# Performance work log

Hardware: AMD Instinct MI355X
Metric: run time of the kernel (lower is better)

## Reference

```python
import jax, jax.numpy as jnp
import numpy as np

N, E, D, L = 20000, 320000, 3072, 64
H = D // 2  # 1536
EPS = 1e-5


def setup_inputs() -> dict:
    key = jax.random.key(0)
    ks = jax.random.split(key, 16)
    inp = {
        "x": jax.random.normal(ks[0], (N, D), dtype=jnp.float32),
        "edge_index": jax.random.randint(ks[1], (2, E), 0, N, dtype=jnp.int64),
        # GCNConv weights (x @ W + b)
        "W_gc1": jax.random.normal(ks[2], (D, H), dtype=jnp.float32) / np.sqrt(D),
        "b_gc1": jnp.zeros((H,), dtype=jnp.float32),
        "W_gc2": jax.random.normal(ks[3], (H, L), dtype=jnp.float32) / np.sqrt(H),
        "b_gc2": jnp.zeros((L,), dtype=jnp.float32),
        # LayerNorm params
        "g1": jnp.ones((H,), dtype=jnp.float32),
        "be1": jnp.zeros((H,), dtype=jnp.float32),
        "g2": jnp.ones((L,), dtype=jnp.float32),
        "be2": jnp.zeros((L,), dtype=jnp.float32),
        # Decoder Linears (PyTorch: y = x @ W.T + b; store as [in, out])
        "W_fc1": jax.random.normal(ks[4], (L, H), dtype=jnp.float32) / np.sqrt(L),
        "b_fc1": jnp.zeros((H,), dtype=jnp.float32),
        "W_fc2": jax.random.normal(ks[5], (H, D), dtype=jnp.float32) / np.sqrt(H),
        "b_fc2": jnp.zeros((D,), dtype=jnp.float32),
    }
    return inp


def _layernorm(h, g, b):
    mu = jnp.mean(h, axis=-1, keepdims=True)
    var = jnp.mean(jnp.square(h - mu), axis=-1, keepdims=True)
    return (h - mu) * jax.lax.rsqrt(var + EPS) * g + b


def _gcn_norm(edge_index, n):
    # PyG GCNConv default: add self-loops, symmetric normalization
    loop = jnp.arange(n, dtype=edge_index.dtype)
    src = jnp.concatenate([edge_index[0], loop])  # [E+N]
    dst = jnp.concatenate([edge_index[1], loop])
    deg = jax.ops.segment_sum(jnp.ones_like(dst, dtype=jnp.float32), dst, num_segments=n)
    dinv = jax.lax.rsqrt(jnp.maximum(deg, 1e-12))
    norm = dinv[src] * dinv[dst]  # [E+N]
    return src, dst, norm


def _gcn_conv(h, W, b, src, dst, norm, n):
    h = h @ W                                 # [N, out]
    m = h[src] * norm[:, None]                # gather + scale over edges
    out = jax.ops.segment_sum(m, dst, num_segments=n)  # scatter-add
    return out + b


def reference(x, edge_index, W_gc1, b_gc1, W_gc2, b_gc2, g1, be1, g2, be2,
              W_fc1, b_fc1, W_fc2, b_fc2):
    n = x.shape[0]
    src, dst, norm = _gcn_norm(edge_index, n)
    hidden = jax.nn.relu(_gcn_conv(x, W_gc1, b_gc1, src, dst, norm, n))
    hidden = _layernorm(hidden, g1, be1)
    latent = jax.nn.relu(_gcn_conv(hidden, W_gc2, b_gc2, src, dst, norm, n))
    latent = _layernorm(latent, g2, be2)
    decode = jax.nn.relu(latent @ W_fc1 + b_fc1)
    reconstructed = decode @ W_fc2 + b_fc2
    return latent, reconstructed
```

## Files before the change

### kernel.cpp

```cpp
#include <hip/hip_runtime.h>
#include <hip/hip_bf16.h>

#define NN 20000
#define EE 320000
#define DD 3072
#define HH 1536
#define LL 64

typedef unsigned short bf16_t;
typedef __attribute__((ext_vector_type(8))) __bf16 bf16x8;
typedef __attribute__((ext_vector_type(4))) float  f32x4;

__device__ __forceinline__ bf16_t f2bf(float f) {
    union { float f; unsigned u; } c; c.f = f;
    unsigned u = c.u;
    return (bf16_t)((u + 0x7fffu + ((u >> 16) & 1u)) >> 16);
}

__global__ void zero_int(int* __restrict__ p, int n) {
    int i = blockIdx.x * blockDim.x + threadIdx.x;
    if (i < n) p[i] = 0;
}

__global__ void cnt_count(const int* __restrict__ ei, int* __restrict__ cnt, int E) {
    int i = blockIdx.x * blockDim.x + threadIdx.x;
    if (i < E) atomicAdd(&cnt[ei[E + i]], 1);
}

__global__ void dinv_from_cnt(const int* __restrict__ cnt, float* __restrict__ dinv, int n) {
    int i = blockIdx.x * blockDim.x + threadIdx.x;
    if (i < n) dinv[i] = rsqrtf((float)(cnt[i] + 1));
}

__global__ __launch_bounds__(1024) void scan_rowptr(const int* __restrict__ cnt,
                                                    int* __restrict__ rowptr, int n)
{
    __shared__ int sdata[1024];
    __shared__ int scarry;
    const int tid = threadIdx.x;
    if (tid == 0) scarry = 0;
    __syncthreads();
    for (int base = 0; base < n; base += 1024) {
        int i = base + tid;
        int v = (i < n) ? cnt[i] : 0;
        int x = v;
        sdata[tid] = x;
        __syncthreads();
#pragma unroll
        for (int off = 1; off < 1024; off <<= 1) {
            int y = (tid >= off) ? sdata[tid - off] : 0;
            __syncthreads();
            x += y;
            sdata[tid] = x;
            __syncthreads();
        }
        if (i < n) rowptr[i] = scarry + x - v;
        int total = sdata[1023];
        __syncthreads();
        if (tid == 0) scarry += total;
        __syncthreads();
    }
    if (tid == 0) rowptr[n] = scarry;
}

__global__ void csr_fill(const int* __restrict__ ei, const int* __restrict__ rowptr,
                         int* __restrict__ cursor, int* __restrict__ csr_src, int E)
{
    int e = blockIdx.x * blockDim.x + threadIdx.x;
    if (e < E) {
        int d = ei[E + e];
        int pos = rowptr[d] + atomicAdd(&cursor[d], 1);
        csr_src[pos] = ei[e];
    }
}

__global__ void cvt_bf16(const float4* __restrict__ in, ushort4* __restrict__ out, long long n4) {
    for (long long i = (long long)blockIdx.x * blockDim.x + threadIdx.x;
         i < n4; i += (long long)gridDim.x * blockDim.x) {
        float4 v = in[i];
        ushort4 o;
        o.x = f2bf(v.x); o.y = f2bf(v.y); o.z = f2bf(v.z); o.w = f2bf(v.w);
        out[i] = o;
    }
}

__global__ __launch_bounds__(256) void cvt_transpose_bf16(
    const float* __restrict__ in, bf16_t* __restrict__ out, int R, int C)
{
    __shared__ float tile[32][33];
    const int bx = blockIdx.x, by = blockIdx.y;
    const int tx = threadIdx.x & 31;
    const int ty = (threadIdx.x >> 5) * 4;
#pragma unroll
    for (int j = 0; j < 4; ++j)
        tile[ty + j][tx] = in[(long long)(by * 32 + ty + j) * C + bx * 32 + tx];
    __syncthreads();
#pragma unroll
    for (int j = 0; j < 4; ++j)
        out[(long long)(bx * 32 + ty + j) * R + by * 32 + tx] = f2bf(tile[tx][ty + j]);
}

#define GLOAD_LDS16(g, l)                                                     \
    __builtin_amdgcn_global_load_lds(                                         \
        (const __attribute__((address_space(1))) unsigned int*)(g),          \
        (__attribute__((address_space(3))) unsigned int*)(l), 16, 0, 0)

#define MFMA16(a, b, c) __builtin_amdgcn_mfma_f32_16x16x32_bf16((a), (b), (c), 0, 0, 0)

#define LDA_F(CUR, MH, MF, KS)                                                \
    (*(const bf16x8*)((const char*)(&lds[(CUR)][0][(MH)][0]) +                \
        (arow + (MF) * 16) * 128 + ((KS) ? offk1 : offk0)))
#define LDB_F(CUR, NH, NF, KS)                                                \
    (*(const bf16x8*)((const char*)(&lds[(CUR)][1][(NH)][0]) +                \
        (brw + (NF) * 16) * 128 + ((KS) ? offk1 : offk0)))

#define READ_AQ(DST, CUR, MH)                                                  \
    _Pragma("unroll")                                                          \
    for (int mf = 0; mf < 4; ++mf) {                                           \
        DST[mf][0] = LDA_F(CUR, MH, mf, 0);                                    \
        DST[mf][1] = LDA_F(CUR, MH, mf, 1);                                    \
    }

#define READ_BQ(DST, CUR, NH)                                                  \
    _Pragma("unroll")                                                          \
    for (int nf = 0; nf < 2; ++nf) {                                           \
        DST[nf][0] = LDB_F(CUR, NH, nf, 0);                                    \
        DST[nf][1] = LDB_F(CUR, NH, nf, 1);                                    \
    }

#define MFMA_Q(MH, NH, PA, PB)                                                 \
    do {                                                                       \
        __builtin_amdgcn_s_setprio(1);                                         \
        _Pragma("unroll")                                                      \
        for (int mf = 0; mf < 4; ++mf) {                                       \
            _Pragma("unroll")                                                  \
            for (int nf = 0; nf < 2; ++nf) {                                   \
                acc[MH][NH][mf][nf] = MFMA16(PA[mf][0], PB[nf][0], acc[MH][NH][mf][nf]); \
                acc[MH][NH][mf][nf] = MFMA16(PA[mf][1], PB[nf][1], acc[MH][NH][mf][nf]); \
            }                                                                  \
        }                                                                      \
        __builtin_amdgcn_s_setprio(0);                                         \
    } while (0)

template <int HAS_BIAS, int RELU, int OUT_BF16>
__global__ __launch_bounds__(512, 2) void gemm_bf16_8ph(
    const bf16_t* __restrict__ A, const bf16_t* __restrict__ Bt,
    const float* __restrict__ bias, void* __restrict__ Cout,
    int M, int N, int K, int gx)
{
    __shared__ bf16_t lds[2][2][2][8192];

    const int nwg = gridDim.x;
    const int q = nwg >> 3, r = nwg & 7;
    const int xcd = blockIdx.x & 7, lo = blockIdx.x >> 3;
    const int wgid = (xcd < r ? xcd * (q + 1) : r * (q + 1) + (xcd - r) * q) + lo;
    const int brow = (wgid / gx) * 256;
    const int bcol = (wgid % gx) * 256;

    const int tid = threadIdx.x;
    const int w = tid >> 6, l = tid & 63;
    const int wr = w >> 2, wc = w & 3;
    const int nt = K >> 6;

    f32x4 acc[2][2][4][2] = {};

    const int srow8 = l >> 3;
    const int swz8  = (((l & 7) ^ (l >> 3)) << 3);

    auto stage_a = [&](int buf, int h, int s) {
#pragma unroll
        for (int i = 0; i < 2; ++i) {
            const int c = (w << 1) + i;
            int grow = brow + h * 128 + c * 8 + srow8;
            if (grow > M - 1) grow = M - 1;
            const bf16_t* g = A + (long long)grow * K + (s << 6) + swz8;
            GLOAD_LDS16(g, &lds[buf][0][h][c * 512]);
        }
    };
    auto stage_b = [&](int buf, int h, int s) {
#pragma unroll
        for (int i = 0; i < 2; ++i) {
            const int c = (w << 1) + i;
            const int grow = bcol + h * 128 + c * 8 + srow8;
            const bf16_t* g = Bt + (long long)grow * K + (s << 6) + swz8;
            GLOAD_LDS16(g, &lds[buf][1][h][c * 512]);
        }
    };

    const int arow  = wr * 64 + (l & 15);
    const int brw   = wc * 32 + (l & 15);
    const int xm    = (l & 7) << 4;
    const int offk0 = ((l >> 4) << 4) ^ xm;
    const int offk1 = (((l >> 4) << 4) + 64) ^ xm;

    stage_a(0, 0, 0); stage_b(0, 0, 0);
    stage_a(0, 1, 0); stage_b(0, 1, 0);
    stage_a(1, 0, 1); stage_b(1, 0, 1);
    __builtin_amdgcn_sched_barrier(0);
    asm volatile("s_waitcnt vmcnt(4)" ::: "memory");
    __builtin_amdgcn_sched_barrier(0);
    __builtin_amdgcn_s_barrier();

    int cur = 0;
    for (int t = 0; t < nt; ++t) {
        const int t1 = (t + 1 < nt) ? t + 1 : nt - 1;
        const int t2 = (t + 2 < nt) ? t + 2 : nt - 1;
        bf16x8 pa0[4][2], pa1[4][2], pb0[2][2], pb1[2][2];

        __builtin_amdgcn_sched_barrier(0);
        READ_AQ(pa0, cur, 0);
        READ_BQ(pb0, cur, 0);
        READ_AQ(pa1, cur, 1);
        stage_a(cur ^ 1, 1, t1);
        MFMA_Q(0, 0, pa0, pb0);
        __builtin_amdgcn_s_barrier();

        __builtin_amdgcn_sched_barrier(0);
        READ_BQ(pb1, cur, 1);
        stage_b(cur ^ 1, 1, t1);
        MFMA_Q(1, 0, pa1, pb0);
        __builtin_amdgcn_s_barrier();

        __builtin_amdgcn_sched_barrier(0);
        stage_a(cur, 0, t2);
        MFMA_Q(1, 1, pa1, pb1);
        __builtin_amdgcn_s_barrier();

        __builtin_amdgcn_sched_barrier(0);
        stage_b(cur, 0, t2);
        MFMA_Q(0, 1, pa0, pb1);
        asm volatile("s_waitcnt vmcnt(4)" ::: "memory");
        __builtin_amdgcn_sched_barrier(0);
        __builtin_amdgcn_s_barrier();

        cur ^= 1;
    }

#pragma unroll
    for (int mh = 0; mh < 2; ++mh) {
#pragma unroll
        for (int nh = 0; nh < 2; ++nh) {
#pragma unroll
            for (int nf = 0; nf < 2; ++nf) {
                const int col = bcol + nh * 128 + wc * 32 + nf * 16 + (l & 15);
                const float bv = HAS_BIAS ? bias[col] : 0.0f;
#pragma unroll
                for (int mf = 0; mf < 4; ++mf) {
#pragma unroll
                    for (int j = 0; j < 4; ++j) {
                        const int row = brow + mh * 128 + wr * 64 + mf * 16 + (l >> 4) * 4 + j;
                        if (row < M) {
                            float v = acc[mh][nh][mf][nf][j] + bv;
                            if (RELU) v = fmaxf(v, 0.0f);
                            if (OUT_BF16) ((bf16_t*)Cout)[(long long)row * N + col] = f2bf(v);
                            else          ((float*)Cout)[(long long)row * N + col] = v;
                        }
                    }
                }
            }
        }
    }
}

template <int HAS_BIAS, int RELU, int OUT_BF16, int BNT>
__global__ __launch_bounds__(256) void gemm_bf16_mfma(
    const bf16_t* __restrict__ A, const bf16_t* __restrict__ Bt,
    const float* __restrict__ bias, void* __restrict__ Cout,
    int M, int N, int K, int gx)
{
    constexpr int NFRAG = BNT / 32;
    constexpr int BHALF = BNT / 64;
    constexpr int WCOFF = BNT / 2;

    __shared__ bf16_t As[128 * 32];
    __shared__ bf16_t Bs[BNT * 32];

    const int nwg = gridDim.x;
    const int q = nwg >> 3, r = nwg & 7;
    const int xcd = blockIdx.x & 7, lo = blockIdx.x >> 3;
    const int wgid = (xcd < r ? xcd * (q + 1) : r * (q + 1) + (xcd - r) * q) + lo;
    const int brow = (wgid / gx) * 128;
    const int bcol = (wgid % gx) * BNT;

    const int tid = threadIdx.x;
    const int w   = tid >> 6;
    const int l   = tid & 63;
    const int wr  = w >> 1, wc = w & 1;

    f32x4 acc[4][NFRAG] = {};

    const int srow   = tid >> 2;
    const int schunk = (tid & 3) * 8;

    for (int k0 = 0; k0 < K; k0 += 32) {
#pragma unroll
        for (int half = 0; half < 2; ++half) {
            int gr = brow + half * 64 + srow;
            if (gr > M - 1) gr = M - 1;
            const bf16_t* gsrc = A + (long long)gr * K + k0 + schunk;
            GLOAD_LDS16(gsrc, &As[(half * 64 + w * 16) * 32]);
        }
#pragma unroll
        for (int half = 0; half < BHALF; ++half) {
            int rr = half * 64 + srow;
            const bf16_t* gsrc = Bt + (long long)(bcol + rr) * K + k0 + schunk;
            GLOAD_LDS16(gsrc, &Bs[(half * 64 + w * 16) * 32]);
        }
        __syncthreads();

        bf16x8 af[4], bfr[NFRAG];
#pragma unroll
        for (int m = 0; m < 4; ++m) {
            int row = wr * 64 + m * 16 + (l & 15);
            af[m] = *(const bf16x8*)&As[row * 32 + (l >> 4) * 8];
        }
#pragma unroll
        for (int n = 0; n < NFRAG; ++n) {
            int row = wc * WCOFF + n * 16 + (l & 15);
            bfr[n] = *(const bf16x8*)&Bs[row * 32 + (l >> 4) * 8];
        }
#pragma unroll
        for (int m = 0; m < 4; ++m)
#pragma unroll
            for (int n = 0; n < NFRAG; ++n)
                acc[m][n] = MFMA16(af[m], bfr[n], acc[m][n]);
        __syncthreads();
    }

#pragma unroll
    for (int m = 0; m < 4; ++m) {
#pragma unroll
        for (int n = 0; n < NFRAG; ++n) {
            int col = bcol + wc * WCOFF + n * 16 + (l & 15);
            float b = HAS_BIAS ? bias[col] : 0.0f;
#pragma unroll
            for (int j = 0; j < 4; ++j) {
                int row = brow + wr * 64 + m * 16 + (l >> 4) * 4 + j;
                if (row < M) {
                    float v = acc[m][n][j] + b;
                    if (RELU) v = fmaxf(v, 0.0f);
                    if (OUT_BF16) ((bf16_t*)Cout)[(long long)row * N + col] = f2bf(v);
                    else          ((float*)Cout)[(long long)row * N + col] = v;
                }
            }
        }
    }
}

__global__ __launch_bounds__(256) void gcn_agg_ln_h(
    const bf16_t* __restrict__ h, const float* __restrict__ dinv,
    const int* __restrict__ rowptr, const int* __restrict__ csr_src,
    const float* __restrict__ bias, const float* __restrict__ g,
    const float* __restrict__ be, bf16_t* __restrict__ out, int n)
{
    const int row  = blockIdx.x * 4 + (threadIdx.x >> 6);
    const int lane = threadIdx.x & 63;
    if (row >= n) return;
    const float dd = dinv[row];

    float acc[24];
    {
        const bf16x8* hr = (const bf16x8*)(h + (long long)row * HH);
#pragma unroll
        for (int c = 0; c < 3; ++c) {
            bf16x8 v = hr[c * 64 + lane];
#pragma unroll
            for (int j = 0; j < 8; ++j) acc[c * 8 + j] = dd * (float)v[j];
        }
    }
    const int s0 = rowptr[row], s1 = rowptr[row + 1];
    for (int k = s0; k < s1; ++k) {
        const int s = csr_src[k];
        const float w = dinv[s];
        const bf16x8* hs = (const bf16x8*)(h + (long long)s * HH);
#pragma unroll
        for (int c = 0; c < 3; ++c) {
            bf16x8 v = hs[c * 64 + lane];
#pragma unroll
            for (int j = 0; j < 8; ++j) acc[c * 8 + j] += w * (float)v[j];
        }
    }

    float lsum = 0.0f, lsq = 0.0f;
#pragma unroll
    for (int c = 0; c < 3; ++c)
#pragma unroll
        for (int j = 0; j < 8; ++j) {
            int idx = c * 512 + lane * 8 + j;
            float v = fmaxf(acc[c * 8 + j] * dd + bias[idx], 0.0f);
            acc[c * 8 + j] = v;
            lsum += v;
            lsq  += v * v;
        }
#pragma unroll
    for (int off = 32; off > 0; off >>= 1) {
        lsum += __shfl_xor(lsum, off);
        lsq  += __shfl_xor(lsq,  off);
    }
    const float mean = lsum / HH;
    const float var  = lsq / HH - mean * mean;
    const float rstd = rsqrtf(var + 1e-5f);

    bf16_t* y = out + (long long)row * HH;
#pragma unroll
    for (int c = 0; c < 3; ++c)
#pragma unroll
        for (int j = 0; j < 8; ++j) {
            int idx = c * 512 + lane * 8 + j;
            y[idx] = f2bf((acc[c * 8 + j] - mean) * rstd * g[idx] + be[idx]);
        }
}

__global__ __launch_bounds__(256) void gcn_agg_ln_l(
    const float* __restrict__ h, const float* __restrict__ dinv,
    const int* __restrict__ rowptr, const int* __restrict__ csr_src,
    const float* __restrict__ bias, const float* __restrict__ g,
    const float* __restrict__ be, float* __restrict__ out,
    bf16_t* __restrict__ outb, int n)
{
    const int row  = blockIdx.x * 4 + (threadIdx.x >> 6);
    const int lane = threadIdx.x & 63;
    if (row >= n) return;
    const float dd = dinv[row];

    float acc = dd * h[(long long)row * LL + lane];
    const int s0 = rowptr[row], s1 = rowptr[row + 1];
    for (int k = s0; k < s1; ++k) {
        const int s = csr_src[k];
        acc += dinv[s] * h[(long long)s * LL + lane];
    }
    float v = fmaxf(acc * dd + bias[lane], 0.0f);
    float lsum = v, lsq = v * v;
#pragma unroll
    for (int off = 32; off > 0; off >>= 1) {
        lsum += __shfl_xor(lsum, off);
        lsq  += __shfl_xor(lsq,  off);
    }
    const float mean = lsum / LL;
    const float var  = lsq / LL - mean * mean;
    const float rstd = rsqrtf(var + 1e-5f);
    float o = (v - mean) * rstd * g[lane] + be[lane];
    out[(long long)row * LL + lane]  = o;
    outb[(long long)row * LL + lane] = f2bf(o);
}

extern "C" void kernel_launch(void* const* d_in, const int* in_sizes, int n_in,
                              void* d_out, int out_size, void* d_ws, size_t ws_size,
                              hipStream_t stream)
{
    const float* x     = (const float*)d_in[0];
    const int*   ei    = (const int*)d_in[1];
    const float* W_gc1 = (const float*)d_in[2];
    const float* b_gc1 = (const float*)d_in[3];
    const float* W_gc2 = (const float*)d_in[4];
    const float* b_gc2 = (const float*)d_in[5];
    const float* g1    = (const float*)d_in[6];
    const float* be1   = (const float*)d_in[7];
    const float* g2    = (const float*)d_in[8];
    const float* be2   = (const float*)d_in[9];
    const float* W_fc1 = (const float*)d_in[10];
    const float* b_fc1 = (const float*)d_in[11];
    const float* W_fc2 = (const float*)d_in[12];
    const float* b_fc2 = (const float*)d_in[13];

    float* out_latent = (float*)d_out;
    float* out_recon  = (float*)d_out + (long long)NN * LL;

    bf16_t* h1b     = (bf16_t*)out_recon;
    bf16_t* hiddenb = (bf16_t*)(out_recon + (long long)NN * HH);

    float*  dinv    = (float*)d_ws;
    int*    cnt     = (int*)(dinv + NN);
    int*    cursor  = cnt + NN;
    int*    rowptr  = cursor + NN;
    int*    csr_src = rowptr + NN + 1;
    char*   pbase   = (char*)(csr_src + EE);
    pbase = (char*)(((size_t)pbase + 255) & ~(size_t)255);
    bf16_t* xb      = (bf16_t*)pbase;
    bf16_t* W1t     = xb + (long long)NN * DD;
    bf16_t* W2t     = W1t + (long long)DD * HH;
    bf16_t* Wg2t    = W2t + (long long)DD * HH;
    bf16_t* Wf1t    = Wg2t + (long long)HH * LL;
    bf16_t* latentb = Wf1t + (long long)LL * HH;
    float*  wsC     = (float*)(latentb + (long long)NN * LL);
    bf16_t* decodeb = xb;

    zero_int<<<(2 * NN + 255) / 256, 256, 0, stream>>>(cnt, 2 * NN);
    cnt_count<<<(EE + 255) / 256, 256, 0, stream>>>(ei, cnt, EE);
    dinv_from_cnt<<<(NN + 255) / 256, 256, 0, stream>>>(cnt, dinv, NN);
    scan_rowptr<<<1, 1024, 0, stream>>>(cnt, rowptr, NN);
    csr_fill<<<(EE + 255) / 256, 256, 0, stream>>>(ei, rowptr, cursor, csr_src, EE);

    cvt_bf16<<<2048, 256, 0, stream>>>((const float4*)x, (ushort4*)xb, (long long)NN * DD / 4);
    {
        dim3 ga(HH / 32, DD / 32);
        cvt_transpose_bf16<<<ga, 256, 0, stream>>>(W_gc1, W1t, DD, HH);
        dim3 gb(DD / 32, HH / 32);
        cvt_transpose_bf16<<<gb, 256, 0, stream>>>(W_fc2, W2t, HH, DD);
        dim3 gc(LL / 32, HH / 32);
        cvt_transpose_bf16<<<gc, 256, 0, stream>>>(W_gc2, Wg2t, HH, LL);
        dim3 gd(HH / 32, LL / 32);
        cvt_transpose_bf16<<<gd, 256, 0, stream>>>(W_fc1, Wf1t, LL, HH);
    }

    const int MB128 = (NN + 127) / 128;
    const int MB256 = (NN + 255) / 256;

    {
        int gx = HH / 256;
        gemm_bf16_8ph<0, 0, 1><<<gx * MB256, 512, 0, stream>>>(xb, W1t, nullptr, h1b, NN, HH, DD, gx);
    }

    gcn_agg_ln_h<<<(NN + 3) / 4, 256, 0, stream>>>(h1b, dinv, rowptr, csr_src, b_gc1, g1, be1, hiddenb, NN);

    gemm_bf16_mfma<0, 0, 0, 64><<<MB128, 256, 0, stream>>>(hiddenb, Wg2t, nullptr, wsC, NN, LL, HH, 1);

    gcn_agg_ln_l<<<(NN + 3) / 4, 256, 0, stream>>>(wsC, dinv, rowptr, csr_src, b_gc2, g2, be2, out_latent, latentb, NN);

    {
        int gx = HH / 128;
        gemm_bf16_mfma<1, 1, 1, 128><<<gx * MB128, 256, 0, stream>>>(latentb, Wf1t, b_fc1, decodeb, NN, HH, LL, gx);
    }

    {
        int gx = DD / 256;
        gemm_bf16_8ph<1, 0, 0><<<gx * MB256, 512, 0, stream>>>(decodeb, W2t, b_fc2, out_recon, NN, DD, HH, gx);
    }
}
```

Measured before the change: 776.5 us.

## Restructure GEMM main-loop barriers and unroll GCN aggregation by two edges

The GEMM main loop drops its sched_barrier fences and splits each quarter-step into LDS reads plus the next global-to-LDS stage, a workgroup barrier, then the MFMA block and a second barrier. The vmcnt wait moves ahead of the last MFMA quarter. Separately, the layer-1 neighbour aggregation now handles two edges per iteration, issuing both rows' loads before accumulating, so more gathers are in flight. The extra barriers add sync overhead and give the compiler freedom to reorder instructions, which may weaken the hand-tuned load/compute interleave. Summing the two edges before adding to the accumulator changes floating-point rounding slightly.

```diff
diff --git a/kernel.cpp b/kernel.cpp
--- a/kernel.cpp
+++ b/kernel.cpp
@@ -196,9 +196,7 @@
     stage_a(0, 0, 0); stage_b(0, 0, 0);
     stage_a(0, 1, 0); stage_b(0, 1, 0);
     stage_a(1, 0, 1); stage_b(1, 0, 1);
-    __builtin_amdgcn_sched_barrier(0);
     asm volatile("s_waitcnt vmcnt(4)" ::: "memory");
-    __builtin_amdgcn_sched_barrier(0);
     __builtin_amdgcn_s_barrier();
 
     int cur = 0;
@@ -207,30 +205,29 @@
         const int t2 = (t + 2 < nt) ? t + 2 : nt - 1;
         bf16x8 pa0[4][2], pa1[4][2], pb0[2][2], pb1[2][2];
 
-        __builtin_amdgcn_sched_barrier(0);
         READ_AQ(pa0, cur, 0);
         READ_BQ(pb0, cur, 0);
+        stage_a(cur ^ 1, 1, t1);
+        __builtin_amdgcn_s_barrier();
+        MFMA_Q(0, 0, pa0, pb0);
+        __builtin_amdgcn_s_barrier();
+
         READ_AQ(pa1, cur, 1);
-        stage_a(cur ^ 1, 1, t1);
-        MFMA_Q(0, 0, pa0, pb0);
-        __builtin_amdgcn_s_barrier();
-
-        __builtin_amdgcn_sched_barrier(0);
+        stage_b(cur ^ 1, 1, t1);
+        __builtin_amdgcn_s_barrier();
+        MFMA_Q(1, 0, pa1, pb0);
+        __builtin_amdgcn_s_barrier();
+
         READ_BQ(pb1, cur, 1);
-        stage_b(cur ^ 1, 1, t1);
-        MFMA_Q(1, 0, pa1, pb0);
-        __builtin_amdgcn_s_barrier();
-
-        __builtin_amdgcn_sched_barrier(0);
         stage_a(cur, 0, t2);
+        __builtin_amdgcn_s_barrier();
         MFMA_Q(1, 1, pa1, pb1);
         __builtin_amdgcn_s_barrier();
 
-        __builtin_amdgcn_sched_barrier(0);
         stage_b(cur, 0, t2);
+        asm volatile("s_waitcnt vmcnt(4)" ::: "memory");
+        __builtin_amdgcn_s_barrier();
         MFMA_Q(0, 1, pa0, pb1);
-        asm volatile("s_waitcnt vmcnt(4)" ::: "memory");
-        __builtin_amdgcn_sched_barrier(0);
         __builtin_amdgcn_s_barrier();
 
         cur ^= 1;
@@ -369,15 +366,32 @@
         }
     }
     const int s0 = rowptr[row], s1 = rowptr[row + 1];
-    for (int k = s0; k < s1; ++k) {
+    int k = s0;
+    for (; k + 1 < s1; k += 2) {
+        const int sa = csr_src[k];
+        const int sb = csr_src[k + 1];
+        const float wa = dinv[sa];
+        const float wb = dinv[sb];
+        const bf16x8* ha = (const bf16x8*)(h + (long long)sa * HH);
+        const bf16x8* hb = (const bf16x8*)(h + (long long)sb * HH);
+        bf16x8 va[3], vb[3];
+#pragma unroll
+        for (int c = 0; c < 3; ++c) { va[c] = ha[c * 64 + lane]; vb[c] = hb[c * 64 + lane]; }
+#pragma unroll
+        for (int c = 0; c < 3; ++c)
+#pragma unroll
+            for (int j = 0; j < 8; ++j)
+                acc[c * 8 + j] += wa * (float)va[c][j] + wb * (float)vb[c][j];
+    }
+    if (k < s1) {
         const int s = csr_src[k];
-        const float w = dinv[s];
+        const float wv = dinv[s];
         const bf16x8* hs = (const bf16x8*)(h + (long long)s * HH);
 #pragma unroll
         for (int c = 0; c < 3; ++c) {
             bf16x8 v = hs[c * 64 + lane];
 #pragma unroll
-            for (int j = 0; j < 8; ++j) acc[c * 8 + j] += w * (float)v[j];
+            for (int j = 0; j < 8; ++j) acc[c * 8 + j] += wv * (float)v[j];
         }
     }
 
```

New measurement: 797.7 us. 1.03x slower.
